# Kernel optimization log

Hardware: AMD Instinct MI355X
Metric: run time of the kernel (lower is better)

The kernel has to match this reference:

```python
import jax, jax.numpy as jnp
import numpy as np


def setup_inputs() -> dict:
    key = jax.random.key(0)
    kq, kk, kv = jax.random.split(key, 3)
    B, L, H, D = 2, 4096, 8, 64
    queries = jax.random.normal(kq, (B, L, H, D), dtype=jnp.float32)
    keys = jax.random.normal(kk, (B, L, H, D), dtype=jnp.float32)
    values = jax.random.normal(kv, (B, L, H, D), dtype=jnp.float32)
    return {"queries": queries, "keys": keys, "values": values}


def reference(queries, keys, values):
    # queries/keys/values: [B, L, H, D]
    d_model = queries.shape[-1]
    scale = 1.0 / jnp.sqrt(jnp.asarray(d_model, dtype=queries.dtype))
    # scores: [B, H, Lq, Lk]
    scores = jnp.einsum('blhd,bshd->bhls', queries, keys)
    # dropout is identity in eval mode / for deterministic reference
    A = jax.nn.softmax(scale * scores, axis=-1)
    # output: [B, Lq, H, D]
    V = jnp.einsum('bhls,bshd->blhd', A, values)
    return V
```

## Files before the change

kernel.cpp:

```cpp
#include <hip/hip_runtime.h>

#define Bn 2
#define Ln 4096
#define Hn 8
#define Dn 64
#define NMEGA 32
#define BH_STRIDE 262144

typedef float    f32x4  __attribute__((ext_vector_type(4)));
typedef float    f32x16 __attribute__((ext_vector_type(16)));
typedef _Float16 f16x2  __attribute__((ext_vector_type(2)));
typedef _Float16 f16x8  __attribute__((ext_vector_type(8)));
typedef unsigned int u32;
typedef u32 u32x2 __attribute__((ext_vector_type(2)));
typedef u32 u32x4 __attribute__((ext_vector_type(4)));

static __device__ __forceinline__ void gld16(const void* g, void* l){
    __builtin_amdgcn_global_load_lds(
        (const __attribute__((address_space(1))) unsigned int*)g,
        (__attribute__((address_space(3))) unsigned int*)l, 16, 0, 0);
}

static __device__ __forceinline__ u32 pkf16(float a, float b){
    auto h = __builtin_amdgcn_cvt_pkrtz(a, b);
    return __builtin_bit_cast(u32, h);
}

static __device__ __forceinline__ u32x2 swp(u32 a, u32 b){
    auto r = __builtin_amdgcn_permlane32_swap(a, b, false, false);
    return __builtin_bit_cast(u32x2, r);
}

__global__ __launch_bounds__(256)
void kvprep(const float* __restrict__ Kg, const float* __restrict__ Vg,
            _Float16* __restrict__ kp, _Float16* __restrict__ vp){
    __shared__ float tile[64*65];
    const int t = blockIdx.x, bh = blockIdx.y, b = bh>>3, h = bh&7;
    const int tid = threadIdx.x;
#pragma unroll
    for(int i=0;i<2;++i){
        int u = tid + i*256;
        int lane = u & 63, unit = u >> 6;
        int g = unit >> 2, cc = unit & 3;
        const float* src = Kg + (((size_t)b*Ln + t*64 + g*32 + (lane&31))*Hn + h)*Dn
                         + cc*16 + (lane>>5)*8;
        float4 a = *(const float4*)src;
        float4 c4 = *(const float4*)(src + 4);
        f16x8 o;
        o[0]=(_Float16)a.x;  o[1]=(_Float16)a.y;  o[2]=(_Float16)a.z;  o[3]=(_Float16)a.w;
        o[4]=(_Float16)c4.x; o[5]=(_Float16)c4.y; o[6]=(_Float16)c4.z; o[7]=(_Float16)c4.w;
        *(f16x8*)(kp + (size_t)bh*BH_STRIDE + (size_t)t*4096 + (size_t)u*8) = o;
    }
#pragma unroll
    for(int i=0;i<4;++i){
        int idx = tid + i*256;
        int k = idx >> 4, d4 = (idx & 15)*4;
        float4 v = *(const float4*)(Vg + (((size_t)b*Ln + t*64 + k)*Hn + h)*Dn + d4);
        tile[k*65 + d4+0]=v.x; tile[k*65 + d4+1]=v.y;
        tile[k*65 + d4+2]=v.z; tile[k*65 + d4+3]=v.w;
    }
    __syncthreads();
#pragma unroll
    for(int i=0;i<2;++i){
        int u = tid + i*256;
        int lane = u & 63, unit = u >> 6;
        int g = unit >> 2, kh = (unit >> 1) & 1, dt = unit & 1;
        int krow = g*32 + kh*16 + (lane>>5)*8;
        int d = dt*32 + (lane&31);
        f16x8 o;
#pragma unroll
        for(int j=0;j<8;++j) o[j] = (_Float16)tile[(krow+j)*65 + d];
        *(f16x8*)(vp + (size_t)bh*BH_STRIDE + (size_t)t*4096 + (size_t)u*8) = o;
    }
}

__global__ __launch_bounds__(256,2)
void attn_fwd(const float* __restrict__ Qg, float* __restrict__ Og,
              const _Float16* __restrict__ kp, const _Float16* __restrict__ vp){
    __shared__ __align__(16) _Float16 sK[2][8192];
    __shared__ __align__(16) _Float16 sV[2][8192];

    const int tid  = threadIdx.x;
    const int lane = tid & 63, wv = tid >> 6;
    const int qh = wv & 1, kh2 = wv >> 1;
    const int l31 = lane & 31, hi = lane >> 5;
    const int bh = blockIdx.x, b = bh>>3, h = bh&7;
    const int q0 = blockIdx.y*128 + qh*64;

    const float c = 0.125f * 1.4426950408889634f;

    f16x8 qf[2][4];
#pragma unroll
    for(int qt=0;qt<2;++qt){
        const float* qrow = Qg + (((size_t)b*Ln + q0 + qt*32 + l31)*Hn + h)*Dn;
#pragma unroll
        for(int cc=0;cc<4;++cc){
            const float* p4 = qrow + cc*16 + hi*8;
            float4 x = *(const float4*)p4;
            float4 y = *(const float4*)(p4+4);
            f16x8 f;
            f[0]=(_Float16)(x.x*c); f[1]=(_Float16)(x.y*c);
            f[2]=(_Float16)(x.z*c); f[3]=(_Float16)(x.w*c);
            f[4]=(_Float16)(y.x*c); f[5]=(_Float16)(y.y*c);
            f[6]=(_Float16)(y.z*c); f[7]=(_Float16)(y.w*c);
            qf[qt][cc]=f;
        }
    }

    f32x16 o[2][2];
    float lac[2] = {0.f, 0.f};
#pragma unroll
    for(int qt=0;qt<2;++qt)
#pragma unroll
        for(int dt=0;dt<2;++dt)
#pragma unroll
            for(int r=0;r<16;++r) o[qt][dt][r]=0.f;

    const _Float16* kg = kp + (size_t)bh*BH_STRIDE;
    const _Float16* vg = vp + (size_t)bh*BH_STRIDE;

    const int kbyte = kh2*8192 + lane*16;

#pragma unroll
    for(int i=0;i<4;++i){
        int u = i*256 + tid;
        gld16(kg + (size_t)u*8, &sK[0][(size_t)u*8]);
        gld16(vg + (size_t)u*8, &sV[0][(size_t)u*8]);
    }

    for(int T=0; T<NMEGA; ++T){
        __syncthreads();
        const int cur = T & 1;
        if(T+1 < NMEGA){
            const int nxt = cur ^ 1;
            const _Float16* kgn = kg + (size_t)(T+1)*8192;
            const _Float16* vgn = vg + (size_t)(T+1)*8192;
#pragma unroll
            for(int i=0;i<4;++i){
                int u = i*256 + tid;
                gld16(kgn + (size_t)u*8, &sK[nxt][(size_t)u*8]);
                gld16(vgn + (size_t)u*8, &sV[nxt][(size_t)u*8]);
            }
        }

#pragma unroll
        for(int g=0; g<2; ++g){
            f16x8 kf[4], vf[2][2];
#pragma unroll
            for(int cc=0;cc<4;++cc)
                kf[cc] = *(const f16x8*)((const char*)&sK[cur][0] + ((g*4+cc)<<10) + kbyte);
#pragma unroll
            for(int kh=0;kh<2;++kh)
#pragma unroll
                for(int dt=0;dt<2;++dt)
                    vf[kh][dt] = *(const f16x8*)((const char*)&sV[cur][0]
                                 + (((g*2+kh)*2+dt)<<10) + kbyte);
#pragma unroll
            for(int qt=0;qt<2;++qt){
                f32x16 s;
#pragma unroll
                for(int r=0;r<16;++r) s[r]=0.f;
                s = __builtin_amdgcn_mfma_f32_32x32x16_f16(kf[0], qf[qt][0], s, 0,0,0);
                s = __builtin_amdgcn_mfma_f32_32x32x16_f16(kf[1], qf[qt][1], s, 0,0,0);
                s = __builtin_amdgcn_mfma_f32_32x32x16_f16(kf[2], qf[qt][2], s, 0,0,0);
                s = __builtin_amdgcn_mfma_f32_32x32x16_f16(kf[3], qf[qt][3], s, 0,0,0);
#pragma unroll
                for(int r=0;r<16;++r) s[r] = __builtin_amdgcn_exp2f(s[r]);
                lac[qt] += ((s[0]+s[1])+(s[2]+s[3])) + ((s[4]+s[5])+(s[6]+s[7]))
                         + ((s[8]+s[9])+(s[10]+s[11])) + ((s[12]+s[13])+(s[14]+s[15]));
                u32 A0 = pkf16(s[0],s[1]),   A1 = pkf16(s[2],s[3]);
                u32 B0 = pkf16(s[4],s[5]),   B1 = pkf16(s[6],s[7]);
                u32 C0 = pkf16(s[8],s[9]),   C1 = pkf16(s[10],s[11]);
                u32 D0 = pkf16(s[12],s[13]), D1 = pkf16(s[14],s[15]);
                u32x2 r0 = swp(A0,B0), r1 = swp(A1,B1);
                u32x2 r2 = swp(C0,D0), r3 = swp(C1,D1);
                u32x4 w0 = {r0.x, r1.x, r0.y, r1.y};
                u32x4 w1 = {r2.x, r3.x, r2.y, r3.y};
                f16x8 pa0 = __builtin_bit_cast(f16x8, w0);
                f16x8 pa1 = __builtin_bit_cast(f16x8, w1);
#pragma unroll
                for(int dt=0;dt<2;++dt){
                    o[qt][dt] = __builtin_amdgcn_mfma_f32_32x32x16_f16(pa0, vf[0][dt], o[qt][dt], 0,0,0);
                    o[qt][dt] = __builtin_amdgcn_mfma_f32_32x32x16_f16(pa1, vf[1][dt], o[qt][dt], 0,0,0);
                }
            }
        }
    }

    float lred[2];
#pragma unroll
    for(int qt=0;qt<2;++qt)
        lred[qt] = lac[qt] + __shfl_xor(lac[qt], 32, 64);

    __syncthreads();
    float* xo = (float*)&sK[0][0];
    float* xl = xo + 128*68;
    if(kh2){
#pragma unroll
        for(int qt=0;qt<2;++qt){
#pragma unroll
            for(int dt=0;dt<2;++dt)
#pragma unroll
                for(int r=0;r<16;++r){
                    int qr = (r&3) + 8*(r>>2) + 4*hi;
                    xo[(qh*64 + qt*32 + qr)*68 + dt*32 + l31] = o[qt][dt][r];
                }
            if(hi==0) xl[qh*64 + qt*32 + l31] = lred[qt];
        }
    }
    __syncthreads();
    if(!kh2){
#pragma unroll
        for(int qt=0;qt<2;++qt){
            float inv = 1.0f/(lred[qt] + xl[qh*64 + qt*32 + l31]);
            float* ob = Og + (((size_t)b*Ln + q0 + qt*32)*Hn + h)*Dn;
#pragma unroll
            for(int r=0;r<16;++r){
                int qr = (r&3) + 8*(r>>2) + 4*hi;
                float invr = __shfl(inv, qr, 64);
#pragma unroll
                for(int dt=0;dt<2;++dt){
                    float val = o[qt][dt][r]
                              + xo[(qh*64 + qt*32 + qr)*68 + dt*32 + l31];
                    ob[(size_t)qr*Hn*Dn + dt*32 + l31] = val*invr;
                }
            }
        }
    }
}

extern "C" void kernel_launch(void* const* d_in, const int* in_sizes, int n_in,
                              void* d_out, int out_size, void* d_ws, size_t ws_size,
                              hipStream_t stream) {
    const float* Q = (const float*)d_in[0];
    const float* K = (const float*)d_in[1];
    const float* V = (const float*)d_in[2];
    float* O = (float*)d_out;

    _Float16* kp = (_Float16*)d_ws;
    _Float16* vp = (_Float16*)((char*)d_ws + (8u<<20));

    kvprep<<<dim3(64, 16), dim3(256), 0, stream>>>(K, V, kp, vp);
    attn_fwd<<<dim3(16, 32), dim3(256), 0, stream>>>(Q, O, kp, vp);
}
```

Baseline: 168.4 us.

## Split attention block into 8 waves with one 32-row query tile each

The attention kernel now launches 512 threads per block. Each of the 8 waves handles one 32-query tile instead of two, cutting per-wave accumulator registers and allowing up to 4 blocks per CU. The K/V tile load is now spread over more threads, and V fragments are read from LDS just before use. The kvprep kernel also stages K through LDS alongside V so both global reads are coalesced float4 row loads. The trade-off is that each K fragment loaded from LDS is reused across fewer query tiles, which raises LDS read traffic per FLOP.

Measured after the change: 175.4 us. 4.1% more time.

```diff
diff --git a/kernel.cpp b/kernel.cpp
--- a/kernel.cpp
+++ b/kernel.cpp
@@ -34,32 +34,35 @@
 __global__ __launch_bounds__(256)
 void kvprep(const float* __restrict__ Kg, const float* __restrict__ Vg,
             _Float16* __restrict__ kp, _Float16* __restrict__ vp){
-    __shared__ float tile[64*65];
+    __shared__ float tK[64*65];
+    __shared__ float tV[64*65];
     const int t = blockIdx.x, bh = blockIdx.y, b = bh>>3, h = bh&7;
     const int tid = threadIdx.x;
+    const size_t rowbase = (((size_t)b*Ln + t*64)*Hn + h)*Dn;
+#pragma unroll
+    for(int i=0;i<4;++i){
+        int idx = tid + i*256;
+        int k = idx >> 4, d4 = (idx & 15)*4;
+        size_t off = rowbase + (size_t)k*Hn*Dn + d4;
+        float4 kv = *(const float4*)(Kg + off);
+        float4 vv = *(const float4*)(Vg + off);
+        tK[k*65+d4+0]=kv.x; tK[k*65+d4+1]=kv.y;
+        tK[k*65+d4+2]=kv.z; tK[k*65+d4+3]=kv.w;
+        tV[k*65+d4+0]=vv.x; tV[k*65+d4+1]=vv.y;
+        tV[k*65+d4+2]=vv.z; tV[k*65+d4+3]=vv.w;
+    }
+    __syncthreads();
 #pragma unroll
     for(int i=0;i<2;++i){
         int u = tid + i*256;
         int lane = u & 63, unit = u >> 6;
         int g = unit >> 2, cc = unit & 3;
-        const float* src = Kg + (((size_t)b*Ln + t*64 + g*32 + (lane&31))*Hn + h)*Dn
-                         + cc*16 + (lane>>5)*8;
-        float4 a = *(const float4*)src;
-        float4 c4 = *(const float4*)(src + 4);
+        int key = g*32 + (lane&31), d0 = cc*16 + (lane>>5)*8;
         f16x8 o;
-        o[0]=(_Float16)a.x;  o[1]=(_Float16)a.y;  o[2]=(_Float16)a.z;  o[3]=(_Float16)a.w;
-        o[4]=(_Float16)c4.x; o[5]=(_Float16)c4.y; o[6]=(_Float16)c4.z; o[7]=(_Float16)c4.w;
+#pragma unroll
+        for(int j=0;j<8;++j) o[j] = (_Float16)tK[key*65 + d0 + j];
         *(f16x8*)(kp + (size_t)bh*BH_STRIDE + (size_t)t*4096 + (size_t)u*8) = o;
     }
-#pragma unroll
-    for(int i=0;i<4;++i){
-        int idx = tid + i*256;
-        int k = idx >> 4, d4 = (idx & 15)*4;
-        float4 v = *(const float4*)(Vg + (((size_t)b*Ln + t*64 + k)*Hn + h)*Dn + d4);
-        tile[k*65 + d4+0]=v.x; tile[k*65 + d4+1]=v.y;
-        tile[k*65 + d4+2]=v.z; tile[k*65 + d4+3]=v.w;
-    }
-    __syncthreads();
 #pragma unroll
     for(int i=0;i<2;++i){
         int u = tid + i*256;
@@ -69,30 +72,28 @@
         int d = dt*32 + (lane&31);
         f16x8 o;
 #pragma unroll
-        for(int j=0;j<8;++j) o[j] = (_Float16)tile[(krow+j)*65 + d];
+        for(int j=0;j<8;++j) o[j] = (_Float16)tV[(krow+j)*65 + d];
         *(f16x8*)(vp + (size_t)bh*BH_STRIDE + (size_t)t*4096 + (size_t)u*8) = o;
     }
 }
 
-__global__ __launch_bounds__(256,2)
+__global__ __launch_bounds__(512,4)
 void attn_fwd(const float* __restrict__ Qg, float* __restrict__ Og,
               const _Float16* __restrict__ kp, const _Float16* __restrict__ vp){
-    __shared__ __align__(16) _Float16 sK[2][8192];
-    __shared__ __align__(16) _Float16 sV[2][8192];
+    __shared__ __align__(16) _Float16 sKV[4][8192];
 
     const int tid  = threadIdx.x;
     const int lane = tid & 63, wv = tid >> 6;
-    const int qh = wv & 1, kh2 = wv >> 1;
+    const int kh2 = wv & 1, qh = wv >> 1;
     const int l31 = lane & 31, hi = lane >> 5;
     const int bh = blockIdx.x, b = bh>>3, h = bh&7;
-    const int q0 = blockIdx.y*128 + qh*64;
+    const int q0 = blockIdx.y*128 + qh*32;
 
     const float c = 0.125f * 1.4426950408889634f;
 
-    f16x8 qf[2][4];
-#pragma unroll
-    for(int qt=0;qt<2;++qt){
-        const float* qrow = Qg + (((size_t)b*Ln + q0 + qt*32 + l31)*Hn + h)*Dn;
+    f16x8 qf[4];
+    {
+        const float* qrow = Qg + (((size_t)b*Ln + q0 + l31)*Hn + h)*Dn;
 #pragma unroll
         for(int cc=0;cc<4;++cc){
             const float* p4 = qrow + cc*16 + hi*8;
@@ -103,18 +104,16 @@
             f[2]=(_Float16)(x.z*c); f[3]=(_Float16)(x.w*c);
             f[4]=(_Float16)(y.x*c); f[5]=(_Float16)(y.y*c);
             f[6]=(_Float16)(y.z*c); f[7]=(_Float16)(y.w*c);
-            qf[qt][cc]=f;
-        }
-    }
-
-    f32x16 o[2][2];
-    float lac[2] = {0.f, 0.f};
-#pragma unroll
-    for(int qt=0;qt<2;++qt)
-#pragma unroll
-        for(int dt=0;dt<2;++dt)
-#pragma unroll
-            for(int r=0;r<16;++r) o[qt][dt][r]=0.f;
+            qf[cc]=f;
+        }
+    }
+
+    f32x16 o[2];
+    float lac = 0.f;
+#pragma unroll
+    for(int dt=0;dt<2;++dt)
+#pragma unroll
+        for(int r=0;r<16;++r) o[dt][r]=0.f;
 
     const _Float16* kg = kp + (size_t)bh*BH_STRIDE;
     const _Float16* vg = vp + (size_t)bh*BH_STRIDE;
@@ -122,10 +121,10 @@
     const int kbyte = kh2*8192 + lane*16;
 
 #pragma unroll
-    for(int i=0;i<4;++i){
-        int u = i*256 + tid;
-        gld16(kg + (size_t)u*8, &sK[0][(size_t)u*8]);
-        gld16(vg + (size_t)u*8, &sV[0][(size_t)u*8]);
+    for(int i=0;i<2;++i){
+        int u = i*512 + tid;
+        gld16(kg + (size_t)u*8, &sKV[0][(size_t)u*8]);
+        gld16(vg + (size_t)u*8, &sKV[2][(size_t)u*8]);
     }
 
     for(int T=0; T<NMEGA; ++T){
@@ -136,94 +135,80 @@
             const _Float16* kgn = kg + (size_t)(T+1)*8192;
             const _Float16* vgn = vg + (size_t)(T+1)*8192;
 #pragma unroll
-            for(int i=0;i<4;++i){
-                int u = i*256 + tid;
-                gld16(kgn + (size_t)u*8, &sK[nxt][(size_t)u*8]);
-                gld16(vgn + (size_t)u*8, &sV[nxt][(size_t)u*8]);
+            for(int i=0;i<2;++i){
+                int u = i*512 + tid;
+                gld16(kgn + (size_t)u*8, &sKV[nxt][(size_t)u*8]);
+                gld16(vgn + (size_t)u*8, &sKV[2+nxt][(size_t)u*8]);
             }
         }
 
 #pragma unroll
         for(int g=0; g<2; ++g){
-            f16x8 kf[4], vf[2][2];
+            f16x8 kf[4];
 #pragma unroll
             for(int cc=0;cc<4;++cc)
-                kf[cc] = *(const f16x8*)((const char*)&sK[cur][0] + ((g*4+cc)<<10) + kbyte);
-#pragma unroll
-            for(int kh=0;kh<2;++kh)
-#pragma unroll
-                for(int dt=0;dt<2;++dt)
-                    vf[kh][dt] = *(const f16x8*)((const char*)&sV[cur][0]
-                                 + (((g*2+kh)*2+dt)<<10) + kbyte);
-#pragma unroll
-            for(int qt=0;qt<2;++qt){
-                f32x16 s;
-#pragma unroll
-                for(int r=0;r<16;++r) s[r]=0.f;
-                s = __builtin_amdgcn_mfma_f32_32x32x16_f16(kf[0], qf[qt][0], s, 0,0,0);
-                s = __builtin_amdgcn_mfma_f32_32x32x16_f16(kf[1], qf[qt][1], s, 0,0,0);
-                s = __builtin_amdgcn_mfma_f32_32x32x16_f16(kf[2], qf[qt][2], s, 0,0,0);
-                s = __builtin_amdgcn_mfma_f32_32x32x16_f16(kf[3], qf[qt][3], s, 0,0,0);
-#pragma unroll
-                for(int r=0;r<16;++r) s[r] = __builtin_amdgcn_exp2f(s[r]);
-                lac[qt] += ((s[0]+s[1])+(s[2]+s[3])) + ((s[4]+s[5])+(s[6]+s[7]))
-                         + ((s[8]+s[9])+(s[10]+s[11])) + ((s[12]+s[13])+(s[14]+s[15]));
-                u32 A0 = pkf16(s[0],s[1]),   A1 = pkf16(s[2],s[3]);
-                u32 B0 = pkf16(s[4],s[5]),   B1 = pkf16(s[6],s[7]);
-                u32 C0 = pkf16(s[8],s[9]),   C1 = pkf16(s[10],s[11]);
-                u32 D0 = pkf16(s[12],s[13]), D1 = pkf16(s[14],s[15]);
-                u32x2 r0 = swp(A0,B0), r1 = swp(A1,B1);
-                u32x2 r2 = swp(C0,D0), r3 = swp(C1,D1);
-                u32x4 w0 = {r0.x, r1.x, r0.y, r1.y};
-                u32x4 w1 = {r2.x, r3.x, r2.y, r3.y};
-                f16x8 pa0 = __builtin_bit_cast(f16x8, w0);
-                f16x8 pa1 = __builtin_bit_cast(f16x8, w1);
-#pragma unroll
-                for(int dt=0;dt<2;++dt){
-                    o[qt][dt] = __builtin_amdgcn_mfma_f32_32x32x16_f16(pa0, vf[0][dt], o[qt][dt], 0,0,0);
-                    o[qt][dt] = __builtin_amdgcn_mfma_f32_32x32x16_f16(pa1, vf[1][dt], o[qt][dt], 0,0,0);
-                }
-            }
-        }
-    }
-
-    float lred[2];
-#pragma unroll
-    for(int qt=0;qt<2;++qt)
-        lred[qt] = lac[qt] + __shfl_xor(lac[qt], 32, 64);
+                kf[cc] = *(const f16x8*)((const char*)&sKV[cur][0] + ((g*4+cc)<<10) + kbyte);
+
+            f32x16 s;
+#pragma unroll
+            for(int r=0;r<16;++r) s[r]=0.f;
+            s = __builtin_amdgcn_mfma_f32_32x32x16_f16(kf[0], qf[0], s, 0,0,0);
+            s = __builtin_amdgcn_mfma_f32_32x32x16_f16(kf[1], qf[1], s, 0,0,0);
+            s = __builtin_amdgcn_mfma_f32_32x32x16_f16(kf[2], qf[2], s, 0,0,0);
+            s = __builtin_amdgcn_mfma_f32_32x32x16_f16(kf[3], qf[3], s, 0,0,0);
+#pragma unroll
+            for(int r=0;r<16;++r) s[r] = __builtin_amdgcn_exp2f(s[r]);
+            lac += ((s[0]+s[1])+(s[2]+s[3])) + ((s[4]+s[5])+(s[6]+s[7]))
+                 + ((s[8]+s[9])+(s[10]+s[11])) + ((s[12]+s[13])+(s[14]+s[15]));
+            u32 A0 = pkf16(s[0],s[1]),   A1 = pkf16(s[2],s[3]);
+            u32 B0 = pkf16(s[4],s[5]),   B1 = pkf16(s[6],s[7]);
+            u32 C0 = pkf16(s[8],s[9]),   C1 = pkf16(s[10],s[11]);
+            u32 D0 = pkf16(s[12],s[13]), D1 = pkf16(s[14],s[15]);
+            u32x2 r0 = swp(A0,B0), r1 = swp(A1,B1);
+            u32x2 r2 = swp(C0,D0), r3 = swp(C1,D1);
+            u32x4 w0 = {r0.x, r1.x, r0.y, r1.y};
+            u32x4 w1 = {r2.x, r3.x, r2.y, r3.y};
+            f16x8 pa0 = __builtin_bit_cast(f16x8, w0);
+            f16x8 pa1 = __builtin_bit_cast(f16x8, w1);
+#pragma unroll
+            for(int dt=0;dt<2;++dt){
+                f16x8 v0 = *(const f16x8*)((const char*)&sKV[2+cur][0]
+                             + (((g*2+0)*2+dt)<<10) + kbyte);
+                f16x8 v1 = *(const f16x8*)((const char*)&sKV[2+cur][0]
+                             + (((g*2+1)*2+dt)<<10) + kbyte);
+                o[dt] = __builtin_amdgcn_mfma_f32_32x32x16_f16(pa0, v0, o[dt], 0,0,0);
+                o[dt] = __builtin_amdgcn_mfma_f32_32x32x16_f16(pa1, v1, o[dt], 0,0,0);
+            }
+        }
+    }
+
+    float lred = lac + __shfl_xor(lac, 32, 64);
 
     __syncthreads();
-    float* xo = (float*)&sK[0][0];
-    float* xl = xo + 128*68;
+    float* xo = (float*)&sKV[0][0];
+    float* xl = xo + 4*32*64;
     if(kh2){
 #pragma unroll
-        for(int qt=0;qt<2;++qt){
-#pragma unroll
-            for(int dt=0;dt<2;++dt)
-#pragma unroll
-                for(int r=0;r<16;++r){
-                    int qr = (r&3) + 8*(r>>2) + 4*hi;
-                    xo[(qh*64 + qt*32 + qr)*68 + dt*32 + l31] = o[qt][dt][r];
-                }
-            if(hi==0) xl[qh*64 + qt*32 + l31] = lred[qt];
-        }
+        for(int dt=0;dt<2;++dt)
+#pragma unroll
+            for(int r=0;r<16;++r){
+                int qr = (r&3) + 8*(r>>2) + 4*hi;
+                xo[(qh*32 + qr)*64 + dt*32 + l31] = o[dt][r];
+            }
+        if(hi==0) xl[qh*32 + l31] = lred;
     }
     __syncthreads();
     if(!kh2){
-#pragma unroll
-        for(int qt=0;qt<2;++qt){
-            float inv = 1.0f/(lred[qt] + xl[qh*64 + qt*32 + l31]);
-            float* ob = Og + (((size_t)b*Ln + q0 + qt*32)*Hn + h)*Dn;
-#pragma unroll
-            for(int r=0;r<16;++r){
-                int qr = (r&3) + 8*(r>>2) + 4*hi;
-                float invr = __shfl(inv, qr, 64);
-#pragma unroll
-                for(int dt=0;dt<2;++dt){
-                    float val = o[qt][dt][r]
-                              + xo[(qh*64 + qt*32 + qr)*68 + dt*32 + l31];
-                    ob[(size_t)qr*Hn*Dn + dt*32 + l31] = val*invr;
-                }
+        float inv = 1.0f/(lred + xl[qh*32 + l31]);
+        float* ob = Og + (((size_t)b*Ln + q0)*Hn + h)*Dn;
+#pragma unroll
+        for(int r=0;r<16;++r){
+            int qr = (r&3) + 8*(r>>2) + 4*hi;
+            float invr = __shfl(inv, qr, 64);
+#pragma unroll
+            for(int dt=0;dt<2;++dt){
+                float val = o[dt][r] + xo[(qh*32 + qr)*64 + dt*32 + l31];
+                ob[(size_t)qr*Hn*Dn + dt*32 + l31] = val*invr;
             }
         }
     }
@@ -241,5 +226,5 @@
     _Float16* vp = (_Float16*)((char*)d_ws + (8u<<20));
 
     kvprep<<<dim3(64, 16), dim3(256), 0, stream>>>(K, V, kp, vp);
-    attn_fwd<<<dim3(16, 32), dim3(256), 0, stream>>>(Q, O, kp, vp);
-}
+    attn_fwd<<<dim3(16, 32), dim3(512), 0, stream>>>(Q, O, kp, vp);
+}
```
